# Optimization experiments

Measured on AMD Instinct MI355X. Metric: run time of the kernel, lower is better.

Reference implementation:

```python
import jax, jax.numpy as jnp
import numpy as np

K, NC, NA = 9, 13, 5
NB, NH, NW = 128, 26, 26
NT, L = 50, 2 * K + 3
NOOBJ, OBJ, SIL = 1.0, 5.0, 0.6
COORD_S, CLASS_S = 1.0, 1.0
PRETRAIN_EPOCHS = 15
TH, SHARP = 80.0, 2.0                      # corner-conf distance threshold (px), sharpness
SCALE = np.array([640.0, 480.0], np.float32)  # im_width, im_height used by corner_confidences
CONF0 = float(np.exp(SHARP) - 1.0)
ANCHORS = np.array([1.482, 2.2412, 2.0501, 3.1265, 2.3946, 4.6891,
                    3.1018, 3.991, 3.4879, 5.8851], np.float32).reshape(NA, 2)


def setup_inputs():
    k1, k2 = jax.random.split(jax.random.key(0))
    output = jax.random.normal(k1, (NB, NA * (2 * K + 1 + NC), NH, NW), dtype=jnp.float32)
    target = jax.random.uniform(k2, (NB, NT * L), dtype=jnp.float32)
    return {"output": output, "target": target, "epoch": 20}


def _corner_conf(pred, gt):
    # pred, gt: [..., K, 2] normalized corners -> mean per-corner confidence [...]
    d = jnp.sqrt((((pred - gt) * jnp.asarray(SCALE)) ** 2).sum(-1))  # pixel distance [..., K]
    c = (jnp.exp(SHARP * (1.0 - d / TH)) - 1.0) / CONF0
    return jnp.where(d < TH, c, 0.0).mean(-1)


def _region_loss(output, target, epoch):
    nAnch, nPix = NA * NH * NW, NH * NW
    tgt = jax.lax.stop_gradient(target).reshape(NB, NT, L)
    out = output.reshape(NB, NA, 2 * K + 1 + NC, NH, NW)
    # keypoint 0 gets sigmoid, the rest are raw offsets
    xs = jnp.concatenate([jax.nn.sigmoid(out[:, :, 0:1]), out[:, :, 2:2 * K:2]], axis=2)  # [B,A,K,H,W]
    ys = jnp.concatenate([jax.nn.sigmoid(out[:, :, 1:2]), out[:, :, 3:2 * K:2]], axis=2)
    conf = jax.nn.sigmoid(out[:, :, 2 * K])                             # [B,A,H,W]
    cls_logits = jnp.transpose(out[:, :, 2 * K + 1:], (0, 1, 3, 4, 2))  # [B,A,H,W,NC]

    gxg = jnp.arange(NW, dtype=jnp.float32)
    gyg = jnp.arange(NH, dtype=jnp.float32)
    px = (jax.lax.stop_gradient(xs) + gxg) / NW            # detached, as torch uses .data
    py = (jax.lax.stop_gradient(ys) + gyg[:, None]) / NH
    # pred corners per anchor cell, flat anchor index = a*H*W + j*W + i -> [B, A*H*W, K, 2]
    pc = jnp.transpose(jnp.stack([px, py], -1), (0, 1, 3, 4, 2, 5)).reshape(NB, nAnch, K, 2)

    gt_xy = tgt[:, :, 1:1 + 2 * K].reshape(NB, NT, K, 2)
    # torch loop breaks at first target with x1 == 0 -> cumulative validity
    valid = jnp.cumprod((tgt[:, :, 1] != 0).astype(jnp.int32), axis=1) > 0  # [B,T]

    # pass 1: max corner confidence over valid GT, per anchor cell
    def max_conf_step(cur, inp):
        gt_t, v_t = inp                                    # [B,K,2], [B]
        c = _corner_conf(pc, gt_t[:, None]).reshape(NB, NA, NH, NW)
        return jnp.where(v_t[:, None, None, None], jnp.maximum(cur, c), cur), None

    cur_confs, _ = jax.lax.scan(max_conf_step, jnp.zeros((NB, NA, NH, NW), jnp.float32),
                                (jnp.swapaxes(gt_xy, 0, 1), valid.T))
    conf_mask0 = jnp.where(cur_confs > SIL, 0.0, NOOBJ)

    # per-target quantities (vectorized over b,t)
    gx = gt_xy[..., 0] * NW                                # [B,T,K]
    gy = gt_xy[..., 1] * NH
    gi0 = jnp.clip(jnp.floor(gx[:, :, 0]).astype(jnp.int32), 0, NW - 1)  # [B,T]
    gj0 = jnp.clip(jnp.floor(gy[:, :, 0]).astype(jnp.int32), 0, NH - 1)
    # pred_box is fetched with best_n == -1 (as in the source); emulate torch negative flat index via mod
    flat_idx = jnp.mod(jnp.arange(NB)[:, None] * nAnch - nPix + gj0 * NW + gi0, NB * nAnch)
    pred_box = pc.reshape(NB * nAnch, K, 2)[flat_idx]      # [B,T,K,2]
    conf_t = _corner_conf(pred_box, gt_xy)                 # [B,T]
    gw = tgt[:, :, L - 2] * NW
    gh = tgt[:, :, L - 1] * NH
    aw, ah = ANCHORS[:, 0], ANCHORS[:, 1]
    mw = jnp.minimum(aw, gw[..., None])                    # centered-box IoU (bbox_iou, cxcywh)
    mh = jnp.minimum(ah, gh[..., None])
    inter = mw * mh
    iou = inter / (aw * ah + (gw * gh)[..., None] - inter)
    best_n = jnp.argmax(iou, axis=-1).astype(jnp.int32)    # [B,T] (first max, like strict '>')
    txv = gx - gi0[..., None].astype(jnp.float32)          # [B,T,K]
    tyv = gy - gj0[..., None].astype(jnp.float32)
    tclsv = tgt[:, :, 0]

    # pass 2: sequential scatter matching torch overwrite order over t
    barange = jnp.arange(NB)
    z = jnp.zeros((NB, NA, NH, NW), jnp.float32)
    zk = jnp.zeros((NB, NA, NH, NW, K), jnp.float32)

    def scatter_step(carry, inp):
        cm, clm, cfm, tx, ty, tcf, tcl = carry
        v, bn, gj, gi, cft, txt, tyt, tct = inp
        idx = (barange, bn, gj, gi)
        vk = v[:, None]
        cm = cm.at[idx].set(jnp.where(v, 1.0, cm[idx]))
        clm = clm.at[idx].set(jnp.where(v, 1.0, clm[idx]))
        cfm = cfm.at[idx].set(jnp.where(v, OBJ, cfm[idx]))
        tx = tx.at[idx].set(jnp.where(vk, txt, tx[idx]))
        ty = ty.at[idx].set(jnp.where(vk, tyt, ty[idx]))
        tcf = tcf.at[idx].set(jnp.where(v, cft, tcf[idx]))
        tcl = tcl.at[idx].set(jnp.where(v, tct, tcl[idx]))
        return (cm, clm, cfm, tx, ty, tcf, tcl), None

    inps = (valid.T, best_n.T, gj0.T, gi0.T, conf_t.T,
            jnp.swapaxes(txv, 0, 1), jnp.swapaxes(tyv, 0, 1), tclsv.T)
    (coord_mask, cls_mask, conf_mask, tx, ty, tconf, tcls), _ = jax.lax.scan(
        scatter_step, (z, z, conf_mask0, zk, zk, z, z), inps)

    # losses
    xsT = jnp.transpose(xs, (0, 1, 3, 4, 2))               # [B,A,H,W,K]
    ysT = jnp.transpose(ys, (0, 1, 3, 4, 2))
    cmk = coord_mask[..., None]
    loss_x = 0.5 * COORD_S * jnp.sum(((xsT - tx) * cmk) ** 2)
    loss_y = 0.5 * COORD_S * jnp.sum(((ysT - ty) * cmk) ** 2)
    sq = jnp.sqrt(conf_mask)
    loss_conf = 0.5 * jnp.sum(((conf - tconf) * sq) ** 2)
    labels = jnp.clip(tcls.astype(jnp.int32), 0, NC - 1)
    ce = -jnp.take_along_axis(jax.nn.log_softmax(cls_logits, axis=-1),
                              labels[..., None], axis=-1)[..., 0]
    loss_cls = CLASS_S * jnp.sum(ce * cls_mask)
    loss = loss_x + loss_y + loss_cls
    if epoch > PRETRAIN_EPOCHS:
        loss = loss + loss_conf
    return loss


def reference(output, target, epoch):
    return _region_loss(output, target, epoch)
```

## Files before the change

### kernel.cpp

```cpp
#include <hip/hip_runtime.h>
#include <math.h>
#include <stdint.h>

#define KK     9
#define NCLS   13
#define NANC   5
#define NBB    128
#define NHH    26
#define NWW    26
#define NTT    50
#define LL     21
#define CHC    32
#define NPIX   676
#define NANCHT 3380
#define NCELLT 432640
#define GTS    20
#define MWPB   106
#define GTH_W  12

#define LOG2E_F   1.4426950408889634f
#define K1C       2.8853900817779268f
#define K2C       0.036067376022224085f
#define SXW       24.615384615384617f
#define SYH       18.461538461538463f
#define THRESH_S  43.500902934225507f
#define CONF_T_SCALE 0.017390849194407297f
#define OBJ_W     5.0f
#define EPOCH_PRETRAIN 15
#define BIGV      6.0e18f

#define CULL_H2   0.36f
#define HSCALE    0.03125f

typedef __attribute__((ext_vector_type(2))) float f2;
typedef __attribute__((ext_vector_type(2))) _Float16 h2;
typedef __attribute__((ext_vector_type(4))) unsigned int u4;
typedef __attribute__((ext_vector_type(2))) unsigned int u2;

static __device__ __forceinline__ float fast_exp2(float x){
  return __builtin_amdgcn_exp2f(x);
}
static __device__ __forceinline__ float fast_sqrt(float x){
  return __builtin_amdgcn_sqrtf(x);
}
static __device__ __forceinline__ float sigmoidf_(float x){
  return 1.0f/(1.0f + fast_exp2(-LOG2E_F*x));
}

static __device__ __forceinline__ u4 sload_u4(const unsigned int* p){
  return *(const __attribute__((address_space(4))) u4*)(uintptr_t)p;
}
static __device__ __forceinline__ u2 sload_u2(const unsigned int* p){
  return *(const __attribute__((address_space(4))) u2*)(uintptr_t)p;
}

__constant__ float c_anch[10] = {1.482f,2.2412f,2.0501f,3.1265f,2.3946f,4.6891f,
                                 3.1018f,3.991f,3.4879f,5.8851f};


__global__ __launch_bounds__(64) void prep_kernel(const float* __restrict__ tgt,
                                                  float* __restrict__ gts_neg,
                                                  unsigned int* __restrict__ gth,
                                                  int* __restrict__ nvalid){
  int b = blockIdx.x;
  int t = threadIdx.x;
  const float* trow = tgt + (size_t)b*NTT*LL;
  float v1 = (t < NTT) ? trow[t*LL + 1] : 0.0f;
  unsigned long long mk = __ballot(t < NTT && v1 != 0.0f);
  int firstInvalid = __ffsll(~mk) - 1;
  if (t == 0) nvalid[b] = firstInvalid;
  for (int idx = t; idx < NTT*GTS; idx += 64){
    int tt = idx / GTS;
    int c  = idx - tt*GTS;
    float v;
    if (c == 9 || c == 19)      v = BIGV;
    else if (c < 9)             v = -(trow[tt*LL + 1 + 2*c] * 640.0f);
    else                        v = -(trow[tt*LL + 2 + 2*(c-10)] * 480.0f);
    gts_neg[(size_t)b*NTT*GTS + idx] = v;
  }
  for (int idx = t; idx < NTT*GTH_W; idx += 64){
    int tt = idx / GTH_W;
    int w  = idx - tt*GTH_W;
    const float* tr2 = trow + tt*LL;
    float a0 = BIGV, a1 = BIGV;
    if (w < 5){
      int k0 = 2*w;
      a0 = -(tr2[1 + 2*k0] * 20.0f);
      if (k0 + 1 < KK) a1 = -(tr2[1 + 2*(k0+1)] * 20.0f);
    } else if (w < 10){
      int k0 = 2*(w-5);
      a0 = -(tr2[2 + 2*k0] * 15.0f);
      if (k0 + 1 < KK) a1 = -(tr2[2 + 2*(k0+1)] * 15.0f);
    }
    h2 hh; hh.x = (_Float16)a0; hh.y = (_Float16)a1;
    gth[(size_t)b*NTT*GTH_W + idx] = __builtin_bit_cast(unsigned int, hh);
  }
}

__global__ __launch_bounds__(256) void region_confmask_kernel(
    const float* __restrict__ outp, const float* __restrict__ gts_neg,
    const unsigned int* __restrict__ gth,
    const int* __restrict__ nvalid, unsigned int* __restrict__ maskw,
    double* __restrict__ partials){
  int b = blockIdx.y;
  int cell = blockIdx.x * blockDim.x + threadIdx.x;
  bool live = (cell < NANCHT);
  int cellc = live ? cell : (NANCHT-1);

  __shared__ float sgt[NTT*GTS] __attribute__((aligned(16)));
  const float* g32 = gts_neg + (size_t)b*NTT*GTS;
  for (int idx = threadIdx.x; idx < NTT*GTS; idx += 256)
    sgt[idx] = g32[idx];
  __syncthreads();

  int a   = cellc / NPIX;
  int rem = cellc - a*NPIX;
  int j   = rem / NWW;
  int i   = rem - j*NWW;
  const float* base = outp + (((size_t)b*NANC + a)*CHC)*NPIX + rem;

  f2 Pxp[5], Pyp[5];
#pragma unroll
  for (int k = 0; k < KK; ++k){
    float rx = base[(2*k)*NPIX];
    float ry = base[(2*k+1)*NPIX];
    if (k == 0){ rx = sigmoidf_(rx); ry = sigmoidf_(ry); }
    Pxp[k>>1][k&1] = (rx + (float)i) * SXW;
    Pyp[k>>1][k&1] = (ry + (float)j) * SYH;
  }
  Pxp[4][1] = 0.0f; Pyp[4][1] = 0.0f;

  h2 Pxh[5], Pyh[5];
#pragma unroll
  for (int p = 0; p < 5; ++p){
    Pxh[p].x = (_Float16)(Pxp[p].x * HSCALE);
    Pxh[p].y = (_Float16)(Pxp[p].y * HSCALE);
    Pyh[p].x = (_Float16)(Pyp[p].x * HSCALE);
    Pyh[p].y = (_Float16)(Pyp[p].y * HSCALE);
  }

  int nv = nvalid[b];
  const unsigned int* gthb = gth + (size_t)b*NTT*GTH_W;
  const _Float16 thh = (_Float16)CULL_H2;
  unsigned long long qbits = 0ull;
#pragma unroll 2
  for (int t = 0; t < nv; ++t){
    u4 q0 = sload_u4(gthb + t*GTH_W);
    u4 q1 = sload_u4(gthb + t*GTH_W + 4);
    u2 q2 = sload_u2(gthb + t*GTH_W + 8);
    h2 Xa[5] = { __builtin_bit_cast(h2, q0.x), __builtin_bit_cast(h2, q0.y),
                 __builtin_bit_cast(h2, q0.z), __builtin_bit_cast(h2, q0.w),
                 __builtin_bit_cast(h2, q1.x) };
    h2 Ya[5] = { __builtin_bit_cast(h2, q1.y), __builtin_bit_cast(h2, q1.z),
                 __builtin_bit_cast(h2, q1.w), __builtin_bit_cast(h2, q2.x),
                 __builtin_bit_cast(h2, q2.y) };
    h2 m2 = {(_Float16)60000.0f, (_Float16)60000.0f};
#pragma unroll
    for (int p = 0; p < 5; ++p){
      h2 dx = Pxh[p] + Xa[p];
      h2 dy = Pyh[p] + Ya[p];
      h2 r  = __builtin_elementwise_fma(dy, dy, dx*dx);
      m2 = __builtin_elementwise_min(m2, r);
    }
    _Float16 mm = (m2.x < m2.y) ? m2.x : m2.y;
    if (mm < thh) qbits |= (1ull << t);
  }

  int m0 = 1;
  if (__any(qbits != 0ull)){
    bool exc = false;
    while (qbits){
      int t = __ffsll((long long)qbits) - 1;
      qbits &= qbits - 1;
      const float* gg = sgt + t*GTS;
      float s = 0.0f;
#pragma unroll
      for (int k = 0; k < KK; ++k){
        float dx = Pxp[k>>1][k&1] + gg[k];
        float dy = Pyp[k>>1][k&1] + gg[10+k];
        float d  = fast_sqrt(fmaf(dy, dy, dx*dx));
        float e  = fast_exp2(fmaf(d, -K2C, K1C));
        s += fmaxf(e, 1.0f);
      }
      exc |= (s > THRESH_S);
    }
    if (exc) m0 = 0;
  }
  float cf = sigmoidf_(base[(2*KK)*NPIX]);
  float contrib = (m0 && live) ? 0.5f*cf*cf : 0.0f;

  unsigned long long mb = __ballot(m0 != 0);
  int lane = threadIdx.x & 63;
  int wavebase = blockIdx.x * 256 + (threadIdx.x & ~63);
  if ((lane & 31) == 0 && wavebase < NANCHT){
    unsigned int w = (lane == 0) ? (unsigned int)mb : (unsigned int)(mb >> 32);
    maskw[(size_t)b*MWPB + (wavebase >> 5) + (lane >> 5)] = w;
  }

#pragma unroll
  for (int o = 32; o > 0; o >>= 1) contrib += __shfl_xor(contrib, o, 64);
  __shared__ float wsum[4];
  int wid = threadIdx.x >> 6;
  if (lane == 0) wsum[wid] = contrib;
  __syncthreads();
  if (threadIdx.x == 0){
    double tot = (double)wsum[0] + (double)wsum[1] + (double)wsum[2] + (double)wsum[3];
    partials[blockIdx.y * gridDim.x + blockIdx.x] = tot;
  }
}

__global__ __launch_bounds__(64) void scatter_loss_kernel(
    const float* __restrict__ outp, const float* __restrict__ tgt,
    const int* __restrict__ nvalid, const unsigned int* __restrict__ maskw,
    double* __restrict__ bc_part){
  int b = blockIdx.x;
  int t = threadIdx.x;
  __shared__ int keys[NTT];
  int nv = nvalid[b];
  bool valid = (t < nv);

  int key = -1, gi0 = 0, gj0 = 0, bn = 0;
  float txv[KK], tyv[KK];
  float conf_t = 0.0f, tcls = 0.0f;

  if (t < NTT){
    const float* trow = tgt + ((size_t)b*NTT + t)*LL;
    tcls = trow[0];
    float gx0 = trow[1]*(float)NWW;
    float gy0 = trow[2]*(float)NHH;
    gi0 = min(max((int)floorf(gx0), 0), NWW-1);
    gj0 = min(max((int)floorf(gy0), 0), NHH-1);
#pragma unroll
    for (int k = 0; k < KK; ++k){
      txv[k] = trow[1+2*k]*(float)NWW - (float)gi0;
      tyv[k] = trow[2+2*k]*(float)NHH - (float)gj0;
    }
    float gw = trow[LL-2]*(float)NWW, gh = trow[LL-1]*(float)NHH;
    float best = -1.0f;
    for (int a = 0; a < NANC; ++a){
      float aw = c_anch[2*a], ah = c_anch[2*a+1];
      float inter = fminf(aw, gw) * fminf(ah, gh);
      float iou = inter / (aw*ah + gw*gh - inter);
      if (iou > best){ best = iou; bn = a; }
    }
    key = bn*NPIX + gj0*NWW + gi0;
    keys[t] = key;

    long f = (long)b*NANCHT - NPIX + gj0*NWW + gi0;
    if (f < 0) f += NCELLT;
    int bb  = (int)(f / NANCHT);
    int rr  = (int)(f - (long)bb*NANCHT);
    int aa  = rr / NPIX;
    int rr2 = rr - aa*NPIX;
    int jj  = rr2 / NWW;
    int ii  = rr2 - jj*NWW;
    const float* pbase = outp + (((size_t)bb*NANC + aa)*CHC)*NPIX + rr2;
    float s = 0.0f;
#pragma unroll
    for (int k = 0; k < KK; ++k){
      float rx = pbase[(2*k)*NPIX], ry = pbase[(2*k+1)*NPIX];
      if (k == 0){ rx = sigmoidf_(rx); ry = sigmoidf_(ry); }
      float Pxx = (rx + (float)ii)*SXW, Pyy = (ry + (float)jj)*SYH;
      float dx = Pxx - trow[1+2*k]*640.0f;
      float dy = Pyy - trow[2+2*k]*480.0f;
      float d  = fast_sqrt(fmaf(dy, dy, dx*dx));
      float e  = fast_exp2(fmaf(d, -K2C, K1C));
      s += fmaxf(e, 1.0f);
    }
    conf_t = (s - 9.0f) * CONF_T_SCALE;
  }
  __syncthreads();

  bool winner = valid;
  if (valid){
    for (int u = t+1; u < nv; ++u) if (keys[u] == key){ winner = false; break; }
  }

  double lx = 0.0, ly = 0.0, lcls = 0.0, lcf = 0.0;
  if (winner){
    const float* cbase = outp + (((size_t)b*NANC + bn)*CHC)*NPIX + gj0*NWW + gi0;
    float sx = 0.0f, sy = 0.0f;
#pragma unroll
    for (int k = 0; k < KK; ++k){
      float rx = cbase[(2*k)*NPIX], ry = cbase[(2*k+1)*NPIX];
      if (k == 0){ rx = sigmoidf_(rx); ry = sigmoidf_(ry); }
      float dx = rx - txv[k], dy = ry - tyv[k];
      sx = fmaf(dx, dx, sx); sy = fmaf(dy, dy, sy);
    }
    lx = 0.5*(double)sx; ly = 0.5*(double)sy;

    float lg[NCLS], mx = -1e30f;
#pragma unroll
    for (int c = 0; c < NCLS; ++c){ lg[c] = cbase[(2*KK+1+c)*NPIX]; mx = fmaxf(mx, lg[c]); }
    float se = 0.0f;
#pragma unroll
    for (int c = 0; c < NCLS; ++c) se += fast_exp2((lg[c]-mx)*LOG2E_F);
    int label = min(max((int)tcls, 0), NCLS-1);
    lcls = (double)(mx + logf(se) - lg[label]);

    float cf = sigmoidf_(cbase[(2*KK)*NPIX]);
    int idx = bn*NPIX + gj0*NWW + gi0;
    int m0 = (maskw[(size_t)b*MWPB + (idx >> 5)] >> (idx & 31)) & 1;
    float dcf = cf - conf_t;
    lcf = 0.5*OBJ_W*(double)(dcf*dcf) - (m0 ? 0.5*(double)(cf*cf) : 0.0);
  }

#pragma unroll
  for (int o = 32; o > 0; o >>= 1){
    lx  += __shfl_xor(lx,  o, 64);
    ly  += __shfl_xor(ly,  o, 64);
    lcls+= __shfl_xor(lcls,o, 64);
    lcf += __shfl_xor(lcf, o, 64);
  }
  if (threadIdx.x == 0){
    double* bp = bc_part + (size_t)b*4;
    bp[0] = lx; bp[1] = ly; bp[2] = lcls; bp[3] = lcf;
  }
}

__global__ __launch_bounds__(256) void finalize_kernel(
    const double* __restrict__ bc_part, const double* __restrict__ partials,
    const int* __restrict__ epoch_p, float* __restrict__ outv){
  int tid = threadIdx.x;
  double vx=0, vy=0, vc=0, vf=0, vb=0;
  for (int i = tid; i < NBB; i += 256){
    vx += bc_part[4*i]; vy += bc_part[4*i+1];
    vc += bc_part[4*i+2]; vf += bc_part[4*i+3];
  }
  for (int i = tid; i < 14*NBB; i += 256) vb += partials[i];
#pragma unroll
  for (int o = 32; o > 0; o >>= 1){
    vx += __shfl_xor(vx, o, 64); vy += __shfl_xor(vy, o, 64);
    vc += __shfl_xor(vc, o, 64); vf += __shfl_xor(vf, o, 64);
    vb += __shfl_xor(vb, o, 64);
  }
  __shared__ double sm[5][4];
  int wid = tid >> 6, lane = tid & 63;
  if (lane == 0){ sm[0][wid]=vx; sm[1][wid]=vy; sm[2][wid]=vc; sm[3][wid]=vf; sm[4][wid]=vb; }
  __syncthreads();
  if (tid == 0){
    double fx=0, fy=0, fc=0, ff=0, fb=0;
    for (int w = 0; w < 4; ++w){ fx+=sm[0][w]; fy+=sm[1][w]; fc+=sm[2][w]; ff+=sm[3][w]; fb+=sm[4][w]; }
    double loss = fx + fy + fc;
    if (*epoch_p > EPOCH_PRETRAIN) loss += ff + fb;
    outv[0] = (float)loss;
  }
}

extern "C" void kernel_launch(void* const* d_in, const int* in_sizes, int n_in,
                              void* d_out, int out_size, void* d_ws, size_t ws_size,
                              hipStream_t stream){
  (void)in_sizes; (void)n_in; (void)out_size; (void)ws_size;
  const float* outp = (const float*)d_in[0];
  const float* tgt  = (const float*)d_in[1];
  const int*   ep   = (const int*)d_in[2];
  float* outv = (float*)d_out;
  char* ws = (char*)d_ws;

  double* bc_part  = (double*)(ws);
  double* partials = (double*)(ws + 4096);
  float*  gts_neg  = (float*) (ws + 18432);
  int*    nvalid   = (int*)   (ws + 530432);
  unsigned int* maskw = (unsigned int*)(ws + 530944);
  unsigned int* gth   = (unsigned int*)(ws + 585216);

  prep_kernel<<<dim3(NBB), dim3(64), 0, stream>>>(tgt, gts_neg, gth, nvalid);
  region_confmask_kernel<<<dim3(14, NBB), dim3(256), 0, stream>>>(outp, gts_neg, gth, nvalid, maskw, partials);
  scatter_loss_kernel<<<dim3(NBB), dim3(64), 0, stream>>>(outp, tgt, nvalid, maskw, bc_part);
  finalize_kernel<<<dim3(1), dim3(256), 0, stream>>>(bc_part, partials, ep, outv);
}
```

Measured before the change: 139.5 us.

## Cull targets by second-smallest corner distance and drop shared-memory GT staging

The half-precision cull test now uses the second-smallest squared corner distance per target instead of the minimum, with a looser threshold. A target is flagged only if at least two corners are close, which is meant to cut the number of exact fp32 confidence evaluations. The shared-memory copy of the GT table and its barrier are removed, so the rare exact path reads global memory directly. The target loop is also unrolled more. Soundness depends on the claim that one close corner cannot push the mean confidence past the threshold, and the fp16 error margin is a risk.

New measurement: 146.0 us. +4.7%, slower.

```diff
diff --git a/kernel.cpp b/kernel.cpp
--- a/kernel.cpp
+++ b/kernel.cpp
@@ -29,7 +29,7 @@
 #define EPOCH_PRETRAIN 15
 #define BIGV      6.0e18f
 
-#define CULL_H2   0.36f
+#define CULL_H2   0.46f
 #define HSCALE    0.03125f
 
 typedef __attribute__((ext_vector_type(2))) float f2;
@@ -52,6 +52,13 @@
 }
 static __device__ __forceinline__ u2 sload_u2(const unsigned int* p){
   return *(const __attribute__((address_space(4))) u2*)(uintptr_t)p;
+}
+
+static __device__ __forceinline__ h2 pk_min_(h2 a, h2 b){
+  return __builtin_elementwise_min(a, b);
+}
+static __device__ __forceinline__ h2 pk_max_(h2 a, h2 b){
+  return __builtin_elementwise_max(a, b);
 }
 
 __constant__ float c_anch[10] = {1.482f,2.2412f,2.0501f,3.1265f,2.3946f,4.6891f,
@@ -107,12 +114,6 @@
   bool live = (cell < NANCHT);
   int cellc = live ? cell : (NANCHT-1);
 
-  __shared__ float sgt[NTT*GTS] __attribute__((aligned(16)));
-  const float* g32 = gts_neg + (size_t)b*NTT*GTS;
-  for (int idx = threadIdx.x; idx < NTT*GTS; idx += 256)
-    sgt[idx] = g32[idx];
-  __syncthreads();
-
   int a   = cellc / NPIX;
   int rem = cellc - a*NPIX;
   int j   = rem / NWW;
@@ -143,7 +144,7 @@
   const unsigned int* gthb = gth + (size_t)b*NTT*GTH_W;
   const _Float16 thh = (_Float16)CULL_H2;
   unsigned long long qbits = 0ull;
-#pragma unroll 2
+#pragma unroll 4
   for (int t = 0; t < nv; ++t){
     u4 q0 = sload_u4(gthb + t*GTH_W);
     u4 q1 = sload_u4(gthb + t*GTH_W + 4);
@@ -154,25 +155,33 @@
     h2 Ya[5] = { __builtin_bit_cast(h2, q1.y), __builtin_bit_cast(h2, q1.z),
                  __builtin_bit_cast(h2, q1.w), __builtin_bit_cast(h2, q2.x),
                  __builtin_bit_cast(h2, q2.y) };
-    h2 m2 = {(_Float16)60000.0f, (_Float16)60000.0f};
+    h2 r[5];
 #pragma unroll
     for (int p = 0; p < 5; ++p){
       h2 dx = Pxh[p] + Xa[p];
       h2 dy = Pyh[p] + Ya[p];
-      h2 r  = __builtin_elementwise_fma(dy, dy, dx*dx);
-      m2 = __builtin_elementwise_min(m2, r);
-    }
-    _Float16 mm = (m2.x < m2.y) ? m2.x : m2.y;
-    if (mm < thh) qbits |= (1ull << t);
+      r[p]  = __builtin_elementwise_fma(dy, dy, dx*dx);
+    }
+    h2 m1a = pk_min_(r[0], r[1]), t1a = pk_max_(r[0], r[1]);
+    h2 m1b = pk_min_(r[2], r[3]), t1b = pk_max_(r[2], r[3]);
+    h2 m1  = pk_min_(m1a, m1b);
+    h2 m2  = pk_min_(pk_max_(m1a, m1b), pk_min_(t1a, t1b));
+    h2 m1f = pk_min_(m1, r[4]);
+    h2 m2f = pk_min_(m2, pk_max_(m1, r[4]));
+    _Float16 hx = (m1f.x > m1f.y) ? m1f.x : m1f.y;
+    _Float16 hm = (m2f.x < m2f.y) ? m2f.x : m2f.y;
+    _Float16 sec = (hx < hm) ? hx : hm;
+    if (sec < thh) qbits |= (1ull << t);
   }
 
   int m0 = 1;
   if (__any(qbits != 0ull)){
     bool exc = false;
+    const float* ggb = gts_neg + (size_t)b*NTT*GTS;
     while (qbits){
       int t = __ffsll((long long)qbits) - 1;
       qbits &= qbits - 1;
-      const float* gg = sgt + t*GTS;
+      const float* gg = ggb + t*GTS;
       float s = 0.0f;
 #pragma unroll
       for (int k = 0; k < KK; ++k){
```

## Split target loop across four waves per 64-cell block with LDS-staged GT halves

Applied to the files above, without the earlier changes.

Each 256-thread block now covers 64 anchor cells instead of 256. Its four waves split the valid-target range four ways, and the per-wave exclusion bits are OR-combined through shared memory before wave 0 writes the mask and the partial sum. The fp16 culling table is staged into LDS rather than read with scalar constant loads. This shortens the serial per-thread target loop and raises grid parallelism, at the cost of four times more blocks, redundant loads of predictions and GT per wave, and an extra barrier.

After: 146.3 us. 4.8% more time.

```diff
diff --git a/kernel.cpp b/kernel.cpp
--- a/kernel.cpp
+++ b/kernel.cpp
@@ -17,6 +17,7 @@
 #define GTS    20
 #define MWPB   106
 #define GTH_W  12
+#define NBLKX  53
 
 #define LOG2E_F   1.4426950408889634f
 #define K1C       2.8853900817779268f
@@ -45,13 +46,6 @@
 }
 static __device__ __forceinline__ float sigmoidf_(float x){
   return 1.0f/(1.0f + fast_exp2(-LOG2E_F*x));
-}
-
-static __device__ __forceinline__ u4 sload_u4(const unsigned int* p){
-  return *(const __attribute__((address_space(4))) u4*)(uintptr_t)p;
-}
-static __device__ __forceinline__ u2 sload_u2(const unsigned int* p){
-  return *(const __attribute__((address_space(4))) u2*)(uintptr_t)p;
 }
 
 __constant__ float c_anch[10] = {1.482f,2.2412f,2.0501f,3.1265f,2.3946f,4.6891f,
@@ -102,15 +96,23 @@
     const unsigned int* __restrict__ gth,
     const int* __restrict__ nvalid, unsigned int* __restrict__ maskw,
     double* __restrict__ partials){
-  int b = blockIdx.y;
-  int cell = blockIdx.x * blockDim.x + threadIdx.x;
+  int b    = blockIdx.y;
+  int lane = threadIdx.x & 63;
+  int w    = threadIdx.x >> 6;
+  int cellbase = blockIdx.x * 64;
+  int cell = cellbase + lane;
   bool live = (cell < NANCHT);
   int cellc = live ? cell : (NANCHT-1);
 
+  __shared__ unsigned int sgh[NTT*GTH_W] __attribute__((aligned(16)));
   __shared__ float sgt[NTT*GTS] __attribute__((aligned(16)));
-  const float* g32 = gts_neg + (size_t)b*NTT*GTS;
-  for (int idx = threadIdx.x; idx < NTT*GTS; idx += 256)
-    sgt[idx] = g32[idx];
+  __shared__ unsigned long long sexcl[4];
+  {
+    const unsigned int* gsrc = gth + (size_t)b*NTT*GTH_W;
+    for (int idx = threadIdx.x; idx < NTT*GTH_W; idx += 256) sgh[idx] = gsrc[idx];
+    const float* fsrc = gts_neg + (size_t)b*NTT*GTS;
+    for (int idx = threadIdx.x; idx < NTT*GTS; idx += 256) sgt[idx] = fsrc[idx];
+  }
   __syncthreads();
 
   int a   = cellc / NPIX;
@@ -140,14 +142,16 @@
   }
 
   int nv = nvalid[b];
-  const unsigned int* gthb = gth + (size_t)b*NTT*GTH_W;
+  int t0 = (w*nv) >> 2;
+  int t1 = ((w+1)*nv) >> 2;
   const _Float16 thh = (_Float16)CULL_H2;
   unsigned long long qbits = 0ull;
 #pragma unroll 2
-  for (int t = 0; t < nv; ++t){
-    u4 q0 = sload_u4(gthb + t*GTH_W);
-    u4 q1 = sload_u4(gthb + t*GTH_W + 4);
-    u2 q2 = sload_u2(gthb + t*GTH_W + 8);
+  for (int t = t0; t < t1; ++t){
+    const u4* q = (const u4*)(sgh + t*GTH_W);
+    u4 q0 = q[0];
+    u4 q1 = q[1];
+    u2 q2 = *(const u2*)(sgh + t*GTH_W + 8);
     h2 Xa[5] = { __builtin_bit_cast(h2, q0.x), __builtin_bit_cast(h2, q0.y),
                  __builtin_bit_cast(h2, q0.z), __builtin_bit_cast(h2, q0.w),
                  __builtin_bit_cast(h2, q1.x) };
@@ -166,9 +170,8 @@
     if (mm < thh) qbits |= (1ull << t);
   }
 
-  int m0 = 1;
+  bool exc = false;
   if (__any(qbits != 0ull)){
-    bool exc = false;
     while (qbits){
       int t = __ffsll((long long)qbits) - 1;
       qbits &= qbits - 1;
@@ -184,28 +187,29 @@
       }
       exc |= (s > THRESH_S);
     }
-    if (exc) m0 = 0;
-  }
-  float cf = sigmoidf_(base[(2*KK)*NPIX]);
-  float contrib = (m0 && live) ? 0.5f*cf*cf : 0.0f;
-
-  unsigned long long mb = __ballot(m0 != 0);
-  int lane = threadIdx.x & 63;
-  int wavebase = blockIdx.x * 256 + (threadIdx.x & ~63);
-  if ((lane & 31) == 0 && wavebase < NANCHT){
-    unsigned int w = (lane == 0) ? (unsigned int)mb : (unsigned int)(mb >> 32);
-    maskw[(size_t)b*MWPB + (wavebase >> 5) + (lane >> 5)] = w;
-  }
-
-#pragma unroll
-  for (int o = 32; o > 0; o >>= 1) contrib += __shfl_xor(contrib, o, 64);
-  __shared__ float wsum[4];
-  int wid = threadIdx.x >> 6;
-  if (lane == 0) wsum[wid] = contrib;
+  }
+
+  unsigned long long em = __ballot(exc);
+  if (lane == 0) sexcl[w] = em;
   __syncthreads();
-  if (threadIdx.x == 0){
-    double tot = (double)wsum[0] + (double)wsum[1] + (double)wsum[2] + (double)wsum[3];
-    partials[blockIdx.y * gridDim.x + blockIdx.x] = tot;
+
+  if (w == 0){
+    unsigned long long finalx = sexcl[0] | sexcl[1] | sexcl[2] | sexcl[3];
+    int m0 = ((finalx >> lane) & 1ull) ? 0 : 1;
+
+    float cf = sigmoidf_(base[(2*KK)*NPIX]);
+    float contrib = (m0 && live) ? 0.5f*cf*cf : 0.0f;
+
+    unsigned long long mb = __ballot(m0 != 0);
+    if ((lane & 31) == 0){
+      unsigned int wv = (lane == 0) ? (unsigned int)mb : (unsigned int)(mb >> 32);
+      maskw[(size_t)b*MWPB + (cellbase >> 5) + (lane >> 5)] = wv;
+    }
+
+#pragma unroll
+    for (int o = 32; o > 0; o >>= 1) contrib += __shfl_xor(contrib, o, 64);
+    if (lane == 0)
+      partials[(size_t)b*NBLKX + blockIdx.x] = (double)contrib;
   }
 }
 
@@ -327,7 +331,7 @@
     vx += bc_part[4*i]; vy += bc_part[4*i+1];
     vc += bc_part[4*i+2]; vf += bc_part[4*i+3];
   }
-  for (int i = tid; i < 14*NBB; i += 256) vb += partials[i];
+  for (int i = tid; i < NBLKX*NBB; i += 256) vb += partials[i];
 #pragma unroll
   for (int o = 32; o > 0; o >>= 1){
     vx += __shfl_xor(vx, o, 64); vy += __shfl_xor(vy, o, 64);
@@ -359,13 +363,13 @@
 
   double* bc_part  = (double*)(ws);
   double* partials = (double*)(ws + 4096);
-  float*  gts_neg  = (float*) (ws + 18432);
-  int*    nvalid   = (int*)   (ws + 530432);
-  unsigned int* maskw = (unsigned int*)(ws + 530944);
-  unsigned int* gth   = (unsigned int*)(ws + 585216);
+  float*  gts_neg  = (float*) (ws + 58368);
+  int*    nvalid   = (int*)   (ws + 570368);
+  unsigned int* maskw = (unsigned int*)(ws + 570880);
+  unsigned int* gth   = (unsigned int*)(ws + 625152);
 
   prep_kernel<<<dim3(NBB), dim3(64), 0, stream>>>(tgt, gts_neg, gth, nvalid);
-  region_confmask_kernel<<<dim3(14, NBB), dim3(256), 0, stream>>>(outp, gts_neg, gth, nvalid, maskw, partials);
+  region_confmask_kernel<<<dim3(NBLKX, NBB), dim3(256), 0, stream>>>(outp, gts_neg, gth, nvalid, maskw, partials);
   scatter_loss_kernel<<<dim3(NBB), dim3(64), 0, stream>>>(outp, tgt, nvalid, maskw, bc_part);
   finalize_kernel<<<dim3(1), dim3(256), 0, stream>>>(bc_part, partials, ep, outv);
 }
```
